# Kernel optimization log

Measured on AMD Instinct MI355X. Metric: run time of the kernel, lower is better.

## Reference

```python
import jax, jax.numpy as jnp
import numpy as np
from jax import lax

B, PN, NS = 8, 16384, 256
KDIM, HID = 512, 384
HALF = HID // 2
EPS = 1e-5


def setup_inputs() -> dict:
    key = jax.random.key(0)
    ks = jax.random.split(key, 12)
    s = lambda fan: np.float32(1.0 / np.sqrt(fan))
    inp = {
        "p": jax.random.normal(ks[0], (B, PN, 3), jnp.float32),
        "N": NS,
        "patch_feature": jax.random.normal(ks[1], (B, KDIM, 1), jnp.float32),
        # Linear(k_dim, hidden)
        "W_feat": jax.random.normal(ks[2], (KDIM, HID), jnp.float32) * s(KDIM),
        "b_feat": jax.random.normal(ks[3], (HID,), jnp.float32) * s(KDIM),
        # Linear(3, hidden//2)
        "W_coord": jax.random.normal(ks[4], (3, HALF), jnp.float32) * s(3),
        "b_coord": jax.random.normal(ks[5], (HALF,), jnp.float32) * s(3),
        # Conv1d(hidden+hidden//2, hidden, 1) == per-point linear, weight (out,in)
        "W1": jax.random.normal(ks[6], (HID, HID + HALF), jnp.float32) * s(HID + HALF),
        "b1": jax.random.normal(ks[7], (HID,), jnp.float32) * s(HID + HALF),
        "g1": jnp.ones((HID,), jnp.float32),
        "be1": jnp.zeros((HID,), jnp.float32),
        # Conv1d(hidden, hidden, 1)
        "W2": jax.random.normal(ks[8], (HID, HID), jnp.float32) * s(HID),
        "b2": jax.random.normal(ks[9], (HID,), jnp.float32) * s(HID),
        "g2": jnp.ones((HID,), jnp.float32),
        "be2": jnp.zeros((HID,), jnp.float32),
    }
    return inp


def farthest_point_sample(points, k):
    """points: (B, N, C) -> (B, k, C). Deterministic start index 0 per batch."""
    b, n, c = points.shape

    def step(carry, _):
        dist, far = carry
        centroid = jnp.take_along_axis(points, far[:, None, None], axis=1)  # (B,1,C)
        d = jnp.sum((points - centroid) ** 2, axis=-1)                      # (B,N)
        dist = jnp.minimum(dist, d)
        new_far = jnp.argmax(dist, axis=-1)
        return (dist, new_far), far

    init = (jnp.full((b, n), 1e10, points.dtype), jnp.zeros((b,), jnp.int32))
    _, idx = lax.scan(step, init, None, length=k)  # idx: (k, B)
    idx = idx.T                                    # (B, k)
    return jnp.take_along_axis(points, idx[:, :, None], axis=1)  # (B,k,C)


def batchnorm(x, gamma, beta):
    """x: (B, L, C); training-mode BN over (B, L) per channel (biased var)."""
    mean = jnp.mean(x, axis=(0, 1))
    var = jnp.var(x, axis=(0, 1))
    return (x - mean) * lax.rsqrt(var + EPS) * gamma + beta


def reference(p, N, patch_feature, W_feat, b_feat, W_coord, b_coord,
              W1, b1, g1, be1, W2, b2, g2, be2):
    b, pn, _ = p.shape
    global_feat = patch_feature[..., 0] @ W_feat + b_feat          # (B, HID)
    global_feat = jnp.broadcast_to(global_feat[:, None, :], (b, N, HID))
    local_feat = p @ W_coord + b_coord                              # (B, PN, HALF)
    if N != pn:
        local_feat = farthest_point_sample(local_feat, N)           # (B, N, HALF)
    combined = jnp.concatenate([global_feat, local_feat], axis=-1)  # (B, N, HID+HALF)
    h = jnp.einsum("bnc,oc->bno", combined, W1) + b1
    h = jax.nn.relu(batchnorm(h, g1, be1))
    h = jnp.einsum("bnc,oc->bno", h, W2) + b2
    h = jax.nn.relu(batchnorm(h, g2, be2))
    return h  # (B, N, HID)
```

## Files before the change

### kernel.cpp

```cpp
#include <hip/hip_runtime.h>

#define BATCH 8
#define PN    16384
#define NSAMP 256
#define KDIM  512
#define HID   384
#define HALF  192
#define CIN   576
#define ROWS  2048
#define BN_EPS 1e-5f

#define OFF_GF   0
#define OFF_W1T  3072
#define OFF_W2T  224256
#define OFF_IDX  371712
#define OFF_H1   373760
#define OFF_H2   1160192
#define OFF_SUM1 1946624
#define OFF_SQ1  1947008
#define OFF_SUM2 1947392
#define OFF_SQ2  1947776

__global__ __launch_bounds__(1024) void k_main(const float* p, const float* Wc,
                                               const float* pf, const float* Wf,
                                               const float* bfe, const float* W1,
                                               const float* W2, float* ws) {
  __shared__ float s[KDIM];
  __shared__ float Msh[6];
  __shared__ unsigned long long red[2][16];
  int blk = blockIdx.x, t = threadIdx.x;

  if (blk >= 8) {
    if (blk < 16) {
      for (int sI = (blk - 8) * 1024 + t; sI < HID * CIN; sI += 8192) {
        int o = sI / CIN, c = sI % CIN;
        ws[OFF_W1T + c * HID + o] = W1[sI];
      }
    } else if (blk < 24) {
      for (int sI = (blk - 16) * 1024 + t; sI < HID * HID; sI += 8192) {
        int o = sI / HID, c = sI % HID;
        ws[OFF_W2T + c * HID + o] = W2[sI];
      }
    } else if (blk < 32) {
      int b = blk - 24;
      if (t < KDIM) s[t] = pf[b * KDIM + t];
      __syncthreads();
      if (t < HID) {
        float acc = bfe[t];
        for (int k = 0; k < KDIM; k++) acc = fmaf(s[k], Wf[k * HID + t], acc);
        ws[OFF_GF + b * HID + t] = acc;
      }
    } else {
      for (int i = t; i < 1536; i += 1024) ws[OFF_SUM1 + i] = 0.f;
    }
    return;
  }

  int b = blk;
  int* idx_out = (int*)(ws + OFF_IDX);

  if (t < 64) {
    double g0 = 0, g1 = 0, g2 = 0, g3 = 0, g4 = 0, g5 = 0;
    for (int k = t; k < HALF; k += 64) {
      double w0 = (double)Wc[k];
      double w1 = (double)Wc[HALF + k];
      double w2 = (double)Wc[2 * HALF + k];
      g0 += w0 * w0; g1 += w0 * w1; g2 += w0 * w2;
      g3 += w1 * w1; g4 += w1 * w2; g5 += w2 * w2;
    }
    for (int off = 32; off; off >>= 1) {
      g0 += __shfl_down(g0, off, 64); g1 += __shfl_down(g1, off, 64);
      g2 += __shfl_down(g2, off, 64); g3 += __shfl_down(g3, off, 64);
      g4 += __shfl_down(g4, off, 64); g5 += __shfl_down(g5, off, 64);
    }
    if (t == 0) {
      double l00 = sqrt(g0);
      double l10 = g1 / l00, l20 = g2 / l00;
      double l11 = sqrt(g3 - l10 * l10);
      double l21 = (g4 - l10 * l20) / l11;
      double l22 = sqrt(g5 - l20 * l20 - l21 * l21);
      Msh[0] = (float)l00; Msh[1] = (float)l10; Msh[2] = (float)l20;
      Msh[3] = (float)l11; Msh[4] = (float)l21; Msh[5] = (float)l22;
    }
  }
  __syncthreads();
  float m00 = Msh[0], m10 = Msh[1], m20 = Msh[2];
  float m11 = Msh[3], m21 = Msh[4], m22 = Msh[5];

  const float* pb = p + b * PN * 3;
  float qx[16], qy[16], qz[16], dist[16];
#pragma unroll
  for (int j = 0; j < 16; j++) {
    int i = (j << 10) + t;
    float x = pb[i * 3], y = pb[i * 3 + 1], z = pb[i * 3 + 2];
    qx[j] = fmaf(m00, x, fmaf(m10, y, m20 * z));
    qy[j] = fmaf(m11, y, m21 * z);
    qz[j] = m22 * z;
    dist[j] = 1e10f;
  }

  int far = 0, par = 0;
  for (int k = 0; k < NSAMP; k++) {
    if (t == 0) idx_out[b * NSAMP + k] = far;
    float x = pb[far * 3], y = pb[far * 3 + 1], z = pb[far * 3 + 2];
    float cx = fmaf(m00, x, fmaf(m10, y, m20 * z));
    float cy = fmaf(m11, y, m21 * z);
    float cz = m22 * z;
    float bv = -1.f; unsigned bj = 0;
#pragma unroll
    for (int j = 0; j < 16; j++) {
      float dx = qx[j] - cx, dy = qy[j] - cy, dz = qz[j] - cz;
      float d  = fmaf(dx, dx, fmaf(dy, dy, dz * dz));
      float nd = fminf(dist[j], d);
      dist[j] = nd;
      bool gt = nd > bv;
      bv = gt ? nd : bv;
      bj = gt ? (unsigned)j : bj;
    }
    unsigned bi = (bj << 10) + (unsigned)t;
    unsigned long long key =
        (((unsigned long long)__float_as_uint(bv)) << 32) | (unsigned)(~bi);
#pragma unroll
    for (int off = 32; off; off >>= 1) {
      unsigned long long o = __shfl_xor(key, off, 64);
      key = (o > key) ? o : key;
    }
    if ((t & 63) == 0) red[par][t >> 6] = key;
    __syncthreads();
    unsigned long long best = red[par][0];
#pragma unroll
    for (int w = 1; w < 16; w++) {
      unsigned long long o = red[par][w];
      best = (o > best) ? o : best;
    }
    far = (int)(~((unsigned)best));
    par ^= 1;
  }
}

__global__ __launch_bounds__(384) void k_gemm1(const float* p,
                                               const float* Wc,
                                               const float* bc,
                                               const float* b1,
                                               float* ws) {
  __shared__ __align__(16) float ct[CIN * 8];
  int t = threadIdx.x;
  int row0 = blockIdx.x * 8;
  const int* fidx = (const int*)(ws + OFF_IDX);
  for (int sI = t; sI < 8 * CIN; sI += 384) {
    int r = sI / CIN, c = sI % CIN;
    int row = row0 + r, b = row >> 8;
    float val;
    if (c < HID) {
      val = ws[OFF_GF + b * HID + c];
    } else {
      int co = c - HID;
      int i = fidx[row];
      const float* pp = p + (b * PN + i) * 3;
      val = bc[co];
      val = fmaf(pp[0], Wc[co], val);
      val = fmaf(pp[1], Wc[HALF + co], val);
      val = fmaf(pp[2], Wc[2 * HALF + co], val);
    }
    ct[c * 8 + r] = val;
  }
  __syncthreads();
  const float* w1t = ws + OFF_W1T;
  float acc[8] = {0.f, 0.f, 0.f, 0.f, 0.f, 0.f, 0.f, 0.f};
  for (int c = 0; c < CIN; c++) {
    float w = w1t[c * HID + t];
    float4 a0 = *(const float4*)(ct + c * 8);
    float4 a1 = *(const float4*)(ct + c * 8 + 4);
    acc[0] = fmaf(a0.x, w, acc[0]); acc[1] = fmaf(a0.y, w, acc[1]);
    acc[2] = fmaf(a0.z, w, acc[2]); acc[3] = fmaf(a0.w, w, acc[3]);
    acc[4] = fmaf(a1.x, w, acc[4]); acc[5] = fmaf(a1.y, w, acc[5]);
    acc[6] = fmaf(a1.z, w, acc[6]); acc[7] = fmaf(a1.w, w, acc[7]);
  }
  float bias = b1[t];
  float sv = 0.f, sq = 0.f;
#pragma unroll
  for (int r = 0; r < 8; r++) {
    float v = acc[r] + bias;
    ws[OFF_H1 + (row0 + r) * HID + t] = v;
    sv += v; sq = fmaf(v, v, sq);
  }
  atomicAdd(&ws[OFF_SUM1 + t], sv);
  atomicAdd(&ws[OFF_SQ1 + t], sq);
}

__global__ __launch_bounds__(384) void k_gemm2(const float* b2,
                                               const float* g1,
                                               const float* be1,
                                               float* ws) {
  __shared__ __align__(16) float ht[HID * 8];
  __shared__ float sc1s[HID], sh1s[HID];
  int t = threadIdx.x;
  int row0 = blockIdx.x * 8;
  {
    float m = ws[OFF_SUM1 + t] * (1.f / ROWS);
    float v = ws[OFF_SQ1 + t] * (1.f / ROWS) - m * m;
    float inv = 1.f / sqrtf(v + BN_EPS);
    float sc = inv * g1[t];
    sc1s[t] = sc;
    sh1s[t] = be1[t] - m * sc;
  }
  __syncthreads();
  for (int sI = t; sI < 8 * HID; sI += 384) {
    int r = sI / HID, c = sI % HID;
    float x = fmaf(ws[OFF_H1 + (row0 + r) * HID + c], sc1s[c], sh1s[c]);
    ht[c * 8 + r] = fmaxf(x, 0.f);
  }
  __syncthreads();
  const float* w2t = ws + OFF_W2T;
  float acc[8] = {0.f, 0.f, 0.f, 0.f, 0.f, 0.f, 0.f, 0.f};
  for (int c = 0; c < HID; c++) {
    float w = w2t[c * HID + t];
    float4 a0 = *(const float4*)(ht + c * 8);
    float4 a1 = *(const float4*)(ht + c * 8 + 4);
    acc[0] = fmaf(a0.x, w, acc[0]); acc[1] = fmaf(a0.y, w, acc[1]);
    acc[2] = fmaf(a0.z, w, acc[2]); acc[3] = fmaf(a0.w, w, acc[3]);
    acc[4] = fmaf(a1.x, w, acc[4]); acc[5] = fmaf(a1.y, w, acc[5]);
    acc[6] = fmaf(a1.z, w, acc[6]); acc[7] = fmaf(a1.w, w, acc[7]);
  }
  float bias = b2[t];
  float sv = 0.f, sq = 0.f;
#pragma unroll
  for (int r = 0; r < 8; r++) {
    float v = acc[r] + bias;
    ws[OFF_H2 + (row0 + r) * HID + t] = v;
    sv += v; sq = fmaf(v, v, sq);
  }
  atomicAdd(&ws[OFF_SUM2 + t], sv);
  atomicAdd(&ws[OFF_SQ2 + t], sq);
}

__global__ __launch_bounds__(256) void k_out(const float* ws, const float* g2,
                                             const float* be2, float* out) {
  int gid = blockIdx.x * 256 + threadIdx.x;
  int i = gid * 4;
  int c = i % HID;
  float4 h  = *(const float4*)(ws + OFF_H2 + i);
  float4 s2 = *(const float4*)(ws + OFF_SUM2 + c);
  float4 q2 = *(const float4*)(ws + OFF_SQ2 + c);
  float4 gv = *(const float4*)(g2 + c);
  float4 bv = *(const float4*)(be2 + c);
  float4 r;
#define BN2(comp) {                                                  \
    float m  = s2.comp * (1.f / ROWS);                               \
    float v  = q2.comp * (1.f / ROWS) - m * m;                       \
    float sc = (1.f / sqrtf(v + BN_EPS)) * gv.comp;                  \
    float sh = bv.comp - m * sc;                                     \
    r.comp = fmaxf(fmaf(h.comp, sc, sh), 0.f); }
  BN2(x) BN2(y) BN2(z) BN2(w)
#undef BN2
  ((float4*)out)[gid] = r;
}

extern "C" void kernel_launch(void* const* d_in, const int* in_sizes, int n_in,
                              void* d_out, int out_size, void* d_ws, size_t ws_size,
                              hipStream_t stream) {
  const float* p   = (const float*)d_in[0];
  const float* pf  = (const float*)d_in[2];
  const float* Wf  = (const float*)d_in[3];
  const float* bfe = (const float*)d_in[4];
  const float* Wc  = (const float*)d_in[5];
  const float* bc  = (const float*)d_in[6];
  const float* W1  = (const float*)d_in[7];
  const float* b1  = (const float*)d_in[8];
  const float* g1  = (const float*)d_in[9];
  const float* be1 = (const float*)d_in[10];
  const float* W2  = (const float*)d_in[11];
  const float* b2  = (const float*)d_in[12];
  const float* g2  = (const float*)d_in[13];
  const float* be2 = (const float*)d_in[14];
  float* ws = (float*)d_ws;

  hipLaunchKernelGGL(k_main,  dim3(33),  dim3(1024), 0, stream,
                     p, Wc, pf, Wf, bfe, W1, W2, ws);
  hipLaunchKernelGGL(k_gemm1, dim3(256), dim3(384), 0, stream, p, Wc, bc, b1, ws);
  hipLaunchKernelGGL(k_gemm2, dim3(256), dim3(384), 0, stream, b2, g1, be1, ws);
  hipLaunchKernelGGL(k_out,   dim3(768), dim3(256), 0, stream,
                     ws, g2, be2, (float*)d_out);
}
```

Before: 599.9 us.

## Fuse all stages into one cooperative kernel with grid-wide syncs

```diff
diff --git a/kernel.cpp b/kernel.cpp
--- a/kernel.cpp
+++ b/kernel.cpp
@@ -1,4 +1,7 @@
 #include <hip/hip_runtime.h>
+#include <hip/hip_cooperative_groups.h>
+
+namespace cg = cooperative_groups;
 
 #define BATCH 8
 #define PN    16384
@@ -21,239 +24,240 @@
 #define OFF_SUM2 1947392
 #define OFF_SQ2  1947776
 
-__global__ __launch_bounds__(1024) void k_main(const float* p, const float* Wc,
-                                               const float* pf, const float* Wf,
-                                               const float* bfe, const float* W1,
-                                               const float* W2, float* ws) {
+__global__ __launch_bounds__(512, 2) void k_all(
+    const float* __restrict__ p,  const float* __restrict__ Wc,
+    const float* __restrict__ bc, const float* __restrict__ pf,
+    const float* __restrict__ Wf, const float* __restrict__ bfe,
+    const float* __restrict__ W1, const float* __restrict__ b1,
+    const float* __restrict__ g1, const float* __restrict__ be1,
+    const float* __restrict__ W2, const float* __restrict__ b2,
+    const float* __restrict__ g2, const float* __restrict__ be2,
+    float* __restrict__ ws, float* __restrict__ out) {
+  cg::grid_group grid = cg::this_grid();
+  int blk = blockIdx.x, t = threadIdx.x;
+
   __shared__ float s[KDIM];
   __shared__ float Msh[6];
-  __shared__ unsigned long long red[2][16];
-  int blk = blockIdx.x, t = threadIdx.x;
-
-  if (blk >= 8) {
-    if (blk < 16) {
-      for (int sI = (blk - 8) * 1024 + t; sI < HID * CIN; sI += 8192) {
-        int o = sI / CIN, c = sI % CIN;
-        ws[OFF_W1T + c * HID + o] = W1[sI];
-      }
-    } else if (blk < 24) {
-      for (int sI = (blk - 16) * 1024 + t; sI < HID * HID; sI += 8192) {
-        int o = sI / HID, c = sI % HID;
-        ws[OFF_W2T + c * HID + o] = W2[sI];
-      }
-    } else if (blk < 32) {
-      int b = blk - 24;
-      if (t < KDIM) s[t] = pf[b * KDIM + t];
+  __shared__ unsigned long long red[2][8];
+  __shared__ __align__(16) float ct[CIN * 8];
+  __shared__ __align__(16) float ht[HID * 8];
+  __shared__ float sA[HID], sB[HID];
+
+  int* idx_out = (int*)(ws + OFF_IDX);
+
+  if (blk < 8) {
+    int b = blk;
+    if (t < 64) {
+      double g0 = 0, g1d = 0, g2d = 0, g3 = 0, g4 = 0, g5 = 0;
+      for (int k = t; k < HALF; k += 64) {
+        double w0 = (double)Wc[k];
+        double w1 = (double)Wc[HALF + k];
+        double w2 = (double)Wc[2 * HALF + k];
+        g0 += w0 * w0; g1d += w0 * w1; g2d += w0 * w2;
+        g3 += w1 * w1; g4  += w1 * w2; g5  += w2 * w2;
+      }
+      for (int off = 32; off; off >>= 1) {
+        g0 += __shfl_down(g0, off, 64); g1d += __shfl_down(g1d, off, 64);
+        g2d += __shfl_down(g2d, off, 64); g3 += __shfl_down(g3, off, 64);
+        g4 += __shfl_down(g4, off, 64); g5 += __shfl_down(g5, off, 64);
+      }
+      if (t == 0) {
+        double l00 = sqrt(g0);
+        double l10 = g1d / l00, l20 = g2d / l00;
+        double l11 = sqrt(g3 - l10 * l10);
+        double l21 = (g4 - l10 * l20) / l11;
+        double l22 = sqrt(g5 - l20 * l20 - l21 * l21);
+        Msh[0] = (float)l00; Msh[1] = (float)l10; Msh[2] = (float)l20;
+        Msh[3] = (float)l11; Msh[4] = (float)l21; Msh[5] = (float)l22;
+      }
+    }
+    __syncthreads();
+    float m00 = Msh[0], m10 = Msh[1], m20 = Msh[2];
+    float m11 = Msh[3], m21 = Msh[4], m22 = Msh[5];
+
+    const float* pb = p + b * PN * 3;
+    float qx[32], qy[32], qz[32], dist[32];
+#pragma unroll
+    for (int j = 0; j < 32; j++) {
+      int i = (j << 9) + t;
+      float x = pb[i * 3], y = pb[i * 3 + 1], z = pb[i * 3 + 2];
+      qx[j] = fmaf(m00, x, fmaf(m10, y, m20 * z));
+      qy[j] = fmaf(m11, y, m21 * z);
+      qz[j] = m22 * z;
+      dist[j] = 1e10f;
+    }
+
+    int far = 0, par = 0;
+    for (int k = 0; k < NSAMP; k++) {
+      if (t == 0) idx_out[b * NSAMP + k] = far;
+      float x = pb[far * 3], y = pb[far * 3 + 1], z = pb[far * 3 + 2];
+      float cx = fmaf(m00, x, fmaf(m10, y, m20 * z));
+      float cy = fmaf(m11, y, m21 * z);
+      float cz = m22 * z;
+      float bv = -1.f; unsigned bj = 0;
+#pragma unroll
+      for (int j = 0; j < 32; j++) {
+        float dx = qx[j] - cx, dy = qy[j] - cy, dz = qz[j] - cz;
+        float d  = fmaf(dx, dx, fmaf(dy, dy, dz * dz));
+        float nd = fminf(dist[j], d);
+        dist[j] = nd;
+        bool gt = nd > bv;
+        bv = gt ? nd : bv;
+        bj = gt ? (unsigned)j : bj;
+      }
+      unsigned bi = (bj << 9) + (unsigned)t;
+      unsigned long long key =
+          (((unsigned long long)__float_as_uint(bv)) << 32) | (unsigned)(~bi);
+#pragma unroll
+      for (int off = 32; off; off >>= 1) {
+        unsigned long long o = __shfl_xor(key, off, 64);
+        key = (o > key) ? o : key;
+      }
+      if ((t & 63) == 0) red[par][t >> 6] = key;
       __syncthreads();
-      if (t < HID) {
-        float acc = bfe[t];
-        for (int k = 0; k < KDIM; k++) acc = fmaf(s[k], Wf[k * HID + t], acc);
-        ws[OFF_GF + b * HID + t] = acc;
-      }
-    } else {
-      for (int i = t; i < 1536; i += 1024) ws[OFF_SUM1 + i] = 0.f;
-    }
-    return;
-  }
-
-  int b = blk;
-  int* idx_out = (int*)(ws + OFF_IDX);
-
-  if (t < 64) {
-    double g0 = 0, g1 = 0, g2 = 0, g3 = 0, g4 = 0, g5 = 0;
-    for (int k = t; k < HALF; k += 64) {
-      double w0 = (double)Wc[k];
-      double w1 = (double)Wc[HALF + k];
-      double w2 = (double)Wc[2 * HALF + k];
-      g0 += w0 * w0; g1 += w0 * w1; g2 += w0 * w2;
-      g3 += w1 * w1; g4 += w1 * w2; g5 += w2 * w2;
-    }
-    for (int off = 32; off; off >>= 1) {
-      g0 += __shfl_down(g0, off, 64); g1 += __shfl_down(g1, off, 64);
-      g2 += __shfl_down(g2, off, 64); g3 += __shfl_down(g3, off, 64);
-      g4 += __shfl_down(g4, off, 64); g5 += __shfl_down(g5, off, 64);
-    }
-    if (t == 0) {
-      double l00 = sqrt(g0);
-      double l10 = g1 / l00, l20 = g2 / l00;
-      double l11 = sqrt(g3 - l10 * l10);
-      double l21 = (g4 - l10 * l20) / l11;
-      double l22 = sqrt(g5 - l20 * l20 - l21 * l21);
-      Msh[0] = (float)l00; Msh[1] = (float)l10; Msh[2] = (float)l20;
-      Msh[3] = (float)l11; Msh[4] = (float)l21; Msh[5] = (float)l22;
-    }
-  }
-  __syncthreads();
-  float m00 = Msh[0], m10 = Msh[1], m20 = Msh[2];
-  float m11 = Msh[3], m21 = Msh[4], m22 = Msh[5];
-
-  const float* pb = p + b * PN * 3;
-  float qx[16], qy[16], qz[16], dist[16];
-#pragma unroll
-  for (int j = 0; j < 16; j++) {
-    int i = (j << 10) + t;
-    float x = pb[i * 3], y = pb[i * 3 + 1], z = pb[i * 3 + 2];
-    qx[j] = fmaf(m00, x, fmaf(m10, y, m20 * z));
-    qy[j] = fmaf(m11, y, m21 * z);
-    qz[j] = m22 * z;
-    dist[j] = 1e10f;
-  }
-
-  int far = 0, par = 0;
-  for (int k = 0; k < NSAMP; k++) {
-    if (t == 0) idx_out[b * NSAMP + k] = far;
-    float x = pb[far * 3], y = pb[far * 3 + 1], z = pb[far * 3 + 2];
-    float cx = fmaf(m00, x, fmaf(m10, y, m20 * z));
-    float cy = fmaf(m11, y, m21 * z);
-    float cz = m22 * z;
-    float bv = -1.f; unsigned bj = 0;
-#pragma unroll
-    for (int j = 0; j < 16; j++) {
-      float dx = qx[j] - cx, dy = qy[j] - cy, dz = qz[j] - cz;
-      float d  = fmaf(dx, dx, fmaf(dy, dy, dz * dz));
-      float nd = fminf(dist[j], d);
-      dist[j] = nd;
-      bool gt = nd > bv;
-      bv = gt ? nd : bv;
-      bj = gt ? (unsigned)j : bj;
-    }
-    unsigned bi = (bj << 10) + (unsigned)t;
-    unsigned long long key =
-        (((unsigned long long)__float_as_uint(bv)) << 32) | (unsigned)(~bi);
-#pragma unroll
-    for (int off = 32; off; off >>= 1) {
-      unsigned long long o = __shfl_xor(key, off, 64);
-      key = (o > key) ? o : key;
-    }
-    if ((t & 63) == 0) red[par][t >> 6] = key;
-    __syncthreads();
-    unsigned long long best = red[par][0];
-#pragma unroll
-    for (int w = 1; w < 16; w++) {
-      unsigned long long o = red[par][w];
-      best = (o > best) ? o : best;
-    }
-    far = (int)(~((unsigned)best));
-    par ^= 1;
-  }
-}
-
-__global__ __launch_bounds__(384) void k_gemm1(const float* p,
-                                               const float* Wc,
-                                               const float* bc,
-                                               const float* b1,
-                                               float* ws) {
-  __shared__ __align__(16) float ct[CIN * 8];
-  int t = threadIdx.x;
-  int row0 = blockIdx.x * 8;
-  const int* fidx = (const int*)(ws + OFF_IDX);
-  for (int sI = t; sI < 8 * CIN; sI += 384) {
-    int r = sI / CIN, c = sI % CIN;
-    int row = row0 + r, b = row >> 8;
-    float val;
-    if (c < HID) {
-      val = ws[OFF_GF + b * HID + c];
-    } else {
-      int co = c - HID;
-      int i = fidx[row];
-      const float* pp = p + (b * PN + i) * 3;
-      val = bc[co];
-      val = fmaf(pp[0], Wc[co], val);
-      val = fmaf(pp[1], Wc[HALF + co], val);
-      val = fmaf(pp[2], Wc[2 * HALF + co], val);
-    }
-    ct[c * 8 + r] = val;
-  }
-  __syncthreads();
-  const float* w1t = ws + OFF_W1T;
-  float acc[8] = {0.f, 0.f, 0.f, 0.f, 0.f, 0.f, 0.f, 0.f};
-  for (int c = 0; c < CIN; c++) {
-    float w = w1t[c * HID + t];
-    float4 a0 = *(const float4*)(ct + c * 8);
-    float4 a1 = *(const float4*)(ct + c * 8 + 4);
-    acc[0] = fmaf(a0.x, w, acc[0]); acc[1] = fmaf(a0.y, w, acc[1]);
-    acc[2] = fmaf(a0.z, w, acc[2]); acc[3] = fmaf(a0.w, w, acc[3]);
-    acc[4] = fmaf(a1.x, w, acc[4]); acc[5] = fmaf(a1.y, w, acc[5]);
-    acc[6] = fmaf(a1.z, w, acc[6]); acc[7] = fmaf(a1.w, w, acc[7]);
-  }
-  float bias = b1[t];
-  float sv = 0.f, sq = 0.f;
-#pragma unroll
-  for (int r = 0; r < 8; r++) {
-    float v = acc[r] + bias;
-    ws[OFF_H1 + (row0 + r) * HID + t] = v;
-    sv += v; sq = fmaf(v, v, sq);
-  }
-  atomicAdd(&ws[OFF_SUM1 + t], sv);
-  atomicAdd(&ws[OFF_SQ1 + t], sq);
-}
-
-__global__ __launch_bounds__(384) void k_gemm2(const float* b2,
-                                               const float* g1,
-                                               const float* be1,
-                                               float* ws) {
-  __shared__ __align__(16) float ht[HID * 8];
-  __shared__ float sc1s[HID], sh1s[HID];
-  int t = threadIdx.x;
-  int row0 = blockIdx.x * 8;
+      unsigned long long k2 = red[par][t & 7];
+#pragma unroll
+      for (int off = 1; off < 8; off <<= 1) {
+        unsigned long long o = __shfl_xor(k2, off, 64);
+        k2 = (o > k2) ? o : k2;
+      }
+      far = __builtin_amdgcn_readfirstlane((int)(~((unsigned)k2)));
+      par ^= 1;
+    }
+  } else if (blk < 16) {
+    for (int sI = (blk - 8) * 512 + t; sI < HID * CIN; sI += 4096) {
+      int o = sI / CIN, c = sI % CIN;
+      ws[OFF_W1T + c * HID + o] = W1[sI];
+    }
+  } else if (blk < 24) {
+    for (int sI = (blk - 16) * 512 + t; sI < HID * HID; sI += 4096) {
+      int o = sI / HID, c = sI % HID;
+      ws[OFF_W2T + c * HID + o] = W2[sI];
+    }
+  } else if (blk < 32) {
+    int b = blk - 24;
+    s[t] = pf[b * KDIM + t];
+    __syncthreads();
+    if (t < HID) {
+      float acc = bfe[t];
+      for (int k = 0; k < KDIM; k++) acc = fmaf(s[k], Wf[k * HID + t], acc);
+      ws[OFF_GF + b * HID + t] = acc;
+    }
+  } else if (blk == 32) {
+    for (int i = t; i < 1536; i += 512) ws[OFF_SUM1 + i] = 0.f;
+  }
+  grid.sync();
+
   {
-    float m = ws[OFF_SUM1 + t] * (1.f / ROWS);
-    float v = ws[OFF_SQ1 + t] * (1.f / ROWS) - m * m;
-    float inv = 1.f / sqrtf(v + BN_EPS);
-    float sc = inv * g1[t];
-    sc1s[t] = sc;
-    sh1s[t] = be1[t] - m * sc;
-  }
-  __syncthreads();
-  for (int sI = t; sI < 8 * HID; sI += 384) {
-    int r = sI / HID, c = sI % HID;
-    float x = fmaf(ws[OFF_H1 + (row0 + r) * HID + c], sc1s[c], sh1s[c]);
-    ht[c * 8 + r] = fmaxf(x, 0.f);
-  }
-  __syncthreads();
-  const float* w2t = ws + OFF_W2T;
-  float acc[8] = {0.f, 0.f, 0.f, 0.f, 0.f, 0.f, 0.f, 0.f};
-  for (int c = 0; c < HID; c++) {
-    float w = w2t[c * HID + t];
-    float4 a0 = *(const float4*)(ht + c * 8);
-    float4 a1 = *(const float4*)(ht + c * 8 + 4);
-    acc[0] = fmaf(a0.x, w, acc[0]); acc[1] = fmaf(a0.y, w, acc[1]);
-    acc[2] = fmaf(a0.z, w, acc[2]); acc[3] = fmaf(a0.w, w, acc[3]);
-    acc[4] = fmaf(a1.x, w, acc[4]); acc[5] = fmaf(a1.y, w, acc[5]);
-    acc[6] = fmaf(a1.z, w, acc[6]); acc[7] = fmaf(a1.w, w, acc[7]);
-  }
-  float bias = b2[t];
-  float sv = 0.f, sq = 0.f;
-#pragma unroll
-  for (int r = 0; r < 8; r++) {
-    float v = acc[r] + bias;
-    ws[OFF_H2 + (row0 + r) * HID + t] = v;
-    sv += v; sq = fmaf(v, v, sq);
-  }
-  atomicAdd(&ws[OFF_SUM2 + t], sv);
-  atomicAdd(&ws[OFF_SQ2 + t], sq);
-}
-
-__global__ __launch_bounds__(256) void k_out(const float* ws, const float* g2,
-                                             const float* be2, float* out) {
-  int gid = blockIdx.x * 256 + threadIdx.x;
-  int i = gid * 4;
-  int c = i % HID;
-  float4 h  = *(const float4*)(ws + OFF_H2 + i);
-  float4 s2 = *(const float4*)(ws + OFF_SUM2 + c);
-  float4 q2 = *(const float4*)(ws + OFF_SQ2 + c);
-  float4 gv = *(const float4*)(g2 + c);
-  float4 bv = *(const float4*)(be2 + c);
-  float4 r;
-#define BN2(comp) {                                                  \
-    float m  = s2.comp * (1.f / ROWS);                               \
-    float v  = q2.comp * (1.f / ROWS) - m * m;                       \
-    float sc = (1.f / sqrtf(v + BN_EPS)) * gv.comp;                  \
-    float sh = bv.comp - m * sc;                                     \
-    r.comp = fmaxf(fmaf(h.comp, sc, sh), 0.f); }
-  BN2(x) BN2(y) BN2(z) BN2(w)
-#undef BN2
-  ((float4*)out)[gid] = r;
+    int row0 = blk * 8;
+    const int* fidx = (const int*)(ws + OFF_IDX);
+    for (int sI = t; sI < 8 * CIN; sI += 512) {
+      int r = sI / CIN, c = sI % CIN;
+      int row = row0 + r, b = row >> 8;
+      float val;
+      if (c < HID) {
+        val = ws[OFF_GF + b * HID + c];
+      } else {
+        int co = c - HID;
+        int i = fidx[row];
+        const float* pp = p + (b * PN + i) * 3;
+        val = bc[co];
+        val = fmaf(pp[0], Wc[co], val);
+        val = fmaf(pp[1], Wc[HALF + co], val);
+        val = fmaf(pp[2], Wc[2 * HALF + co], val);
+      }
+      ct[c * 8 + r] = val;
+    }
+    __syncthreads();
+    if (t < HID) {
+      const float* w1t = ws + OFF_W1T;
+      float acc[8] = {0.f, 0.f, 0.f, 0.f, 0.f, 0.f, 0.f, 0.f};
+      for (int c = 0; c < CIN; c++) {
+        float w = w1t[c * HID + t];
+        float4 a0 = *(const float4*)(ct + c * 8);
+        float4 a1 = *(const float4*)(ct + c * 8 + 4);
+        acc[0] = fmaf(a0.x, w, acc[0]); acc[1] = fmaf(a0.y, w, acc[1]);
+        acc[2] = fmaf(a0.z, w, acc[2]); acc[3] = fmaf(a0.w, w, acc[3]);
+        acc[4] = fmaf(a1.x, w, acc[4]); acc[5] = fmaf(a1.y, w, acc[5]);
+        acc[6] = fmaf(a1.z, w, acc[6]); acc[7] = fmaf(a1.w, w, acc[7]);
+      }
+      float bias = b1[t];
+      float sv = 0.f, sq = 0.f;
+#pragma unroll
+      for (int r = 0; r < 8; r++) {
+        float v = acc[r] + bias;
+        ws[OFF_H1 + (row0 + r) * HID + t] = v;
+        sv += v; sq = fmaf(v, v, sq);
+      }
+      atomicAdd(&ws[OFF_SUM1 + t], sv);
+      atomicAdd(&ws[OFF_SQ1 + t], sq);
+    }
+  }
+  grid.sync();
+
+  {
+    int row0 = blk * 8;
+    if (t < HID) {
+      float m = ws[OFF_SUM1 + t] * (1.f / ROWS);
+      float v = ws[OFF_SQ1 + t] * (1.f / ROWS) - m * m;
+      float sc = (1.f / sqrtf(v + BN_EPS)) * g1[t];
+      sA[t] = sc;
+      sB[t] = be1[t] - m * sc;
+    }
+    __syncthreads();
+    for (int sI = t; sI < 8 * HID; sI += 512) {
+      int r = sI / HID, c = sI % HID;
+      float x = fmaf(ws[OFF_H1 + (row0 + r) * HID + c], sA[c], sB[c]);
+      ht[c * 8 + r] = fmaxf(x, 0.f);
+    }
+    __syncthreads();
+    if (t < HID) {
+      const float* w2t = ws + OFF_W2T;
+      float acc[8] = {0.f, 0.f, 0.f, 0.f, 0.f, 0.f, 0.f, 0.f};
+      for (int c = 0; c < HID; c++) {
+        float w = w2t[c * HID + t];
+        float4 a0 = *(const float4*)(ht + c * 8);
+        float4 a1 = *(const float4*)(ht + c * 8 + 4);
+        acc[0] = fmaf(a0.x, w, acc[0]); acc[1] = fmaf(a0.y, w, acc[1]);
+        acc[2] = fmaf(a0.z, w, acc[2]); acc[3] = fmaf(a0.w, w, acc[3]);
+        acc[4] = fmaf(a1.x, w, acc[4]); acc[5] = fmaf(a1.y, w, acc[5]);
+        acc[6] = fmaf(a1.z, w, acc[6]); acc[7] = fmaf(a1.w, w, acc[7]);
+      }
+      float bias = b2[t];
+      float sv = 0.f, sq = 0.f;
+#pragma unroll
+      for (int r = 0; r < 8; r++) {
+        float v = acc[r] + bias;
+        ws[OFF_H2 + (row0 + r) * HID + t] = v;
+        sv += v; sq = fmaf(v, v, sq);
+      }
+      atomicAdd(&ws[OFF_SUM2 + t], sv);
+      atomicAdd(&ws[OFF_SQ2 + t], sq);
+    }
+  }
+  grid.sync();
+
+  {
+    if (t < HID) {
+      float m = ws[OFF_SUM2 + t] * (1.f / ROWS);
+      float v = ws[OFF_SQ2 + t] * (1.f / ROWS) - m * m;
+      float sc = (1.f / sqrtf(v + BN_EPS)) * g2[t];
+      sA[t] = sc;
+      sB[t] = be2[t] - m * sc;
+    }
+    __syncthreads();
+    for (int i4 = blk * 512 + t; i4 < ROWS * HID / 4; i4 += 256 * 512) {
+      int i = i4 * 4;
+      int c = i % HID;
+      float4 h = *(const float4*)(ws + OFF_H2 + i);
+      float4 r;
+      r.x = fmaxf(fmaf(h.x, sA[c],     sB[c]),     0.f);
+      r.y = fmaxf(fmaf(h.y, sA[c + 1], sB[c + 1]), 0.f);
+      r.z = fmaxf(fmaf(h.z, sA[c + 2], sB[c + 2]), 0.f);
+      r.w = fmaxf(fmaf(h.w, sA[c + 3], sB[c + 3]), 0.f);
+      ((float4*)out)[i4] = r;
+    }
+  }
 }
 
 extern "C" void kernel_launch(void* const* d_in, const int* in_sizes, int n_in,
@@ -273,12 +277,12 @@
   const float* b2  = (const float*)d_in[12];
   const float* g2  = (const float*)d_in[13];
   const float* be2 = (const float*)d_in[14];
-  float* ws = (float*)d_ws;
-
-  hipLaunchKernelGGL(k_main,  dim3(33),  dim3(1024), 0, stream,
-                     p, Wc, pf, Wf, bfe, W1, W2, ws);
-  hipLaunchKernelGGL(k_gemm1, dim3(256), dim3(384), 0, stream, p, Wc, bc, b1, ws);
-  hipLaunchKernelGGL(k_gemm2, dim3(256), dim3(384), 0, stream, b2, g1, be1, ws);
-  hipLaunchKernelGGL(k_out,   dim3(768), dim3(256), 0, stream,
-                     ws, g2, be2, (float*)d_out);
+  float* ws  = (float*)d_ws;
+  float* out = (float*)d_out;
+
+  void* args[] = {(void*)&p,  (void*)&Wc, (void*)&bc,  (void*)&pf,
+                  (void*)&Wf, (void*)&bfe,(void*)&W1,  (void*)&b1,
+                  (void*)&g1, (void*)&be1,(void*)&W2,  (void*)&b2,
+                  (void*)&g2, (void*)&be2,(void*)&ws,  (void*)&out};
+  hipLaunchCooperativeKernel((void*)k_all, dim3(256), dim3(512), args, 0, stream);
 }
```

Measured after the change: 613.8 us. 2.3% more time.
